# Kernel optimization log

Hardware: AMD Instinct MI355X
Metric: run time of the kernel (lower is better)

The kernel has to match this reference:

```python
import jax, jax.numpy as jnp
import numpy as np

NUM_TOKENS_SCORE = 64
NUM_HEADS = 16
NUM_KV_HEADS = 4
HEAD_SIZE = 128
SCALE = 0.08838834764831845  # 1/sqrt(128)


def setup_inputs() -> dict:
    key = jax.random.key(0)
    k1, k2, k3 = jax.random.split(key, 3)
    B, S = 2, 2048
    total = B * S
    return {
        "query": jax.random.normal(k1, (total, NUM_HEADS * HEAD_SIZE), dtype=jnp.float32),
        "key": jax.random.normal(k2, (total, NUM_KV_HEADS * HEAD_SIZE), dtype=jnp.float32),
        "value": jax.random.normal(k3, (total, NUM_KV_HEADS * HEAD_SIZE), dtype=jnp.float32),
        "batch_size": B,
        "seq_len": S,
    }


def reference(query, key, value, batch_size, seq_len):
    """Prompt-phase SparsePagedAttention: varlen causal GQA attention (equal
    prompt lengths -> dense [B,S] layout) plus the fused softmax score-sum over
    the last NUM_TOKENS_SCORE query rows used for KV-cache pruning."""
    B, S = batch_size, seq_len
    H, Hk, D = NUM_HEADS, NUM_KV_HEADS, HEAD_SIZE
    rep = H // Hk  # queries per kv head (head_mapping via repeat_interleave)

    q = query.reshape(B, S, H, D)
    k = jnp.repeat(key.reshape(B, S, Hk, D), rep, axis=2)    # [B,S,H,D]
    v = jnp.repeat(value.reshape(B, S, Hk, D), rep, axis=2)  # [B,S,H,D]

    scores = jnp.einsum('bqhd,bkhd->bhqk', q, k) * SCALE      # [B,H,S,S]
    causal = jnp.tril(jnp.ones((S, S), dtype=bool))
    scores = jnp.where(causal[None, None], scores, jnp.finfo(scores.dtype).min)
    probs = jax.nn.softmax(scores, axis=-1)                   # [B,H,S,S]

    out = jnp.einsum('bhqk,bkhd->bqhd', probs, v).reshape(B * S, H * D)
    # triton_fused_softmax_sum: sum softmax probs over last NUM_TOKENS_SCORE queries
    score_sum = probs[:, :, S - NUM_TOKENS_SCORE:, :].sum(axis=2)  # [B,H,S]
    return out, score_sum
```

## Files before the change

### kernel.cpp

```cpp
#include <hip/hip_runtime.h>


#define BB 2
#define SS 2048
#define NH 16
#define NKV 4
#define DD 128
#define TILE_SH 4096

typedef __attribute__((ext_vector_type(8))) short bf16x8;
typedef __attribute__((ext_vector_type(4))) float f32x4;

constexpr float SCL = 0.08838834764831845f * 1.4426950408889634f;

__device__ __forceinline__ short f2bf(float f) {
  union { float f; unsigned u; } v; v.f = f;
  unsigned r = v.u + 0x7FFFu + ((v.u >> 16) & 1u);
  return (short)(r >> 16);
}

__device__ __forceinline__ unsigned pack2bf(float a, float b) {
  union { float f; unsigned u; } x, y; x.f = a; y.f = b;
  return __builtin_amdgcn_perm(y.u, x.u, 0x07060302);
}

__device__ __forceinline__ void gl_lds16(const void* g, void* l) {
  __builtin_amdgcn_global_load_lds(
      (const __attribute__((address_space(1))) unsigned*)g,
      (__attribute__((address_space(3))) unsigned*)l, 16, 0, 0);
}

__global__ void prep(const float* __restrict__ K, const float* __restrict__ V,
                     short* __restrict__ Kb, short* __restrict__ Vb) {
  const int p = blockIdx.x;
  const int b = p >> 8, hk = (p >> 6) & 3, kt = p & 63;
  const int tid = threadIdx.x;
  const int k0 = kt * 32;
  short* kb = Kb + ((size_t)((b * 4 + hk) * 64 + kt)) * TILE_SH;
  short* vb = Vb + ((size_t)((b * 4 + hk) * 64 + kt)) * TILE_SH;
  {
    const int k = tid & 31, chb = tid >> 5;
    const float* src = K + ((size_t)(b * SS + k0 + k) * NKV + hk) * DD;
#pragma unroll
    for (int i = 0; i < 2; ++i) {
      const int ch = chb + i * 8;
      const float* s = src + ch * 8;
      float4 f0 = *(const float4*)s;
      float4 f1 = *(const float4*)(s + 4);
      bf16x8 t;
      t[0] = f2bf(f0.x); t[1] = f2bf(f0.y); t[2] = f2bf(f0.z); t[3] = f2bf(f0.w);
      t[4] = f2bf(f1.x); t[5] = f2bf(f1.y); t[6] = f2bf(f1.z); t[7] = f2bf(f1.w);
      *(bf16x8*)(kb + (ch * 32 + k) * 8) = t;
    }
  }
  {
    const int d = tid & 127, kcb = tid >> 7;
#pragma unroll
    for (int i = 0; i < 2; ++i) {
      const int kc = kcb + i * 2;
      const float* s = V + ((size_t)(b * SS + k0 + kc * 8) * NKV + hk) * DD + d;
      bf16x8 t;
#pragma unroll
      for (int e = 0; e < 8; ++e) t[e] = f2bf(s[(size_t)e * (NKV * DD)]);
      *(bf16x8*)(vb + (kc * 128 + d) * 8) = t;
    }
  }
}

__global__ __launch_bounds__(256, 4) void fa2(
    const float* __restrict__ Q, const short* __restrict__ Kb,
    const short* __restrict__ Vb, float* __restrict__ Out,
    float* __restrict__ wsl) {
  __shared__ bf16x8 kv[2][1024];
  __shared__ short ldsP[4][640];

  const int tid = threadIdx.x;
  const int w = tid >> 6, lane = tid & 63;
  const int c = lane & 15, qd = lane >> 4;

  const int i = blockIdx.x;
  const int g = i >> 8, cc = i & 255;
  const int bh = cc >> 3, jp = cc & 7;
  const int qt = (g == 0) ? jp : (g == 1) ? 31 - jp : (g == 2) ? 8 + jp : 23 - jp;
  const int b = bh >> 4, h = bh & 15, hk = h >> 2;

  const char* KT = (const char*)(Kb + ((size_t)(b * 4 + hk)) * 64 * TILE_SH);
  const char* VT = (const char*)(Vb + ((size_t)(b * 4 + hk)) * 64 * TILE_SH);

  auto stage = [&](int kt, int bi) {
    const char* sk = KT + (size_t)kt * 8192 + w * 2048 + lane * 16;
    const char* sv = VT + (size_t)kt * 8192 + w * 2048 + lane * 16;
    char* dk = (char*)kv[bi] + w * 2048;
    char* dv = dk + 8192;
#pragma unroll
    for (int t = 0; t < 2; ++t) {
      gl_lds16(sk + t * 1024, dk + t * 1024);
      gl_lds16(sv + t * 1024, dv + t * 1024);
    }
  };

  stage(0, 0);

  const int nk = 2 * qt + 2;

  const float* qrow = Q + ((size_t)(b * SS + qt * 64 + w * 16 + c) * NH + h) * DD;
  bf16x8 qf[4];
#pragma unroll
  for (int ks = 0; ks < 4; ++ks) {
    const float* p = qrow + ks * 32 + qd * 8;
    float4 f0 = *(const float4*)p;
    float4 f1 = *(const float4*)(p + 4);
    bf16x8 t;
    t[0] = f2bf(f0.x * SCL); t[1] = f2bf(f0.y * SCL);
    t[2] = f2bf(f0.z * SCL); t[3] = f2bf(f0.w * SCL);
    t[4] = f2bf(f1.x * SCL); t[5] = f2bf(f1.y * SCL);
    t[6] = f2bf(f1.z * SCL); t[7] = f2bf(f1.w * SCL);
    qf[ks] = t;
  }

  f32x4 o[8];
#pragma unroll
  for (int dt = 0; dt < 8; ++dt) { o[dt][0] = 0.f; o[dt][1] = 0.f; o[dt][2] = 0.f; o[dt][3] = 0.f; }
  float l_part = 0.f;

  for (int kt = 0; kt < nk; ++kt) {
    __syncthreads();
    const int cb = kt & 1;
    if (kt + 1 < nk) stage(kt + 1, cb ^ 1);

    const bf16x8* bK = kv[cb];
    const bf16x8* bV = kv[cb] + 512;

    f32x4 st0 = {0.f, 0.f, 0.f, 0.f}, st1 = {0.f, 0.f, 0.f, 0.f};
#pragma unroll
    for (int ks = 0; ks < 4; ++ks) {
      const int chz = (ks * 4 + qd) * 32;
      bf16x8 a0 = bK[chz + c];
      bf16x8 a1 = bK[chz + 16 + c];
      st0 = __builtin_amdgcn_mfma_f32_16x16x32_bf16(a0, qf[ks], st0, 0, 0, 0);
      st1 = __builtin_amdgcn_mfma_f32_16x16x32_bf16(a1, qf[ks], st1, 0, 0, 0);
    }

    float pr[8];
#pragma unroll
    for (int r = 0; r < 4; ++r) { pr[r] = exp2f(st0[r]); pr[4 + r] = exp2f(st1[r]); }
    const int koff = kt * 32 - qt * 64;
    if (koff >= 0) {
      const int qrl = w * 16 + c;
#pragma unroll
      for (int mt = 0; mt < 2; ++mt)
#pragma unroll
        for (int r = 0; r < 4; ++r)
          if (koff + mt * 16 + qd * 4 + r > qrl) pr[mt * 4 + r] = 0.f;
    }
#pragma unroll
    for (int x = 0; x < 8; ++x) l_part += pr[x];

    short* pp = ldsP[w] + c * 40;
#pragma unroll
    for (int mt = 0; mt < 2; ++mt) {
      union { short4 s4; unsigned u[2]; } pk;
      pk.u[0] = pack2bf(pr[mt * 4 + 0], pr[mt * 4 + 1]);
      pk.u[1] = pack2bf(pr[mt * 4 + 2], pr[mt * 4 + 3]);
      *(short4*)(pp + mt * 16 + qd * 4) = pk.s4;
    }
    __asm__ volatile("s_waitcnt lgkmcnt(0)" ::: "memory");
    bf16x8 pf = *(const bf16x8*)(pp + qd * 8);

#pragma unroll
    for (int dt = 0; dt < 8; ++dt)
      o[dt] = __builtin_amdgcn_mfma_f32_16x16x32_bf16(bV[qd * 128 + dt * 16 + c],
                                                      pf, o[dt], 0, 0, 0);
  }

  float l = l_part;
  l += __shfl_xor(l, 16);
  l += __shfl_xor(l, 32);
  const float linv = 1.f / l;

  float* orow = Out + ((size_t)(b * SS + qt * 64 + w * 16 + c) * NH + h) * DD;
#pragma unroll
  for (int dt = 0; dt < 8; ++dt) {
    float4 ov;
    ov.x = o[dt][0] * linv; ov.y = o[dt][1] * linv;
    ov.z = o[dt][2] * linv; ov.w = o[dt][3] * linv;
    *(float4*)(orow + dt * 16 + qd * 4) = ov;
  }
  if (qt == 31 && qd == 0)
    wsl[bh * 64 + w * 16 + c] = l;
}

__global__ __launch_bounds__(256, 2) void score(
    const float* __restrict__ Q, const short* __restrict__ Kb,
    const float* __restrict__ wsl, float* __restrict__ out2) {
  __shared__ float ldsS[4][64];
  const int tid = threadIdx.x;
  const int w = tid >> 6, lane = tid & 63;
  const int c = lane & 15, qd = lane >> 4;
  const int bh = blockIdx.x & 31, kt = blockIdx.x >> 5;
  const int b = bh >> 4, h = bh & 15, hk = h >> 2;
  const int q0 = SS - 64;

  const float* qrow = Q + ((size_t)(b * SS + q0 + w * 16 + c) * NH + h) * DD;
  bf16x8 qf[4];
#pragma unroll
  for (int ks = 0; ks < 4; ++ks) {
    const float* p = qrow + ks * 32 + qd * 8;
    float4 f0 = *(const float4*)p;
    float4 f1 = *(const float4*)(p + 4);
    bf16x8 t;
    t[0] = f2bf(f0.x * SCL); t[1] = f2bf(f0.y * SCL);
    t[2] = f2bf(f0.z * SCL); t[3] = f2bf(f0.w * SCL);
    t[4] = f2bf(f1.x * SCL); t[5] = f2bf(f1.y * SCL);
    t[6] = f2bf(f1.z * SCL); t[7] = f2bf(f1.w * SCL);
    qf[ks] = t;
  }
  float linv[4];
  const int r0 = bh * 64 + w * 16 + qd * 4;
#pragma unroll
  for (int r = 0; r < 4; ++r) linv[r] = 1.f / wsl[r0 + r];

  const bf16x8* kb = (const bf16x8*)Kb + ((size_t)(b * 4 + hk) * 64 + kt * 2) * 512;
  f32x4 s[4];
#pragma unroll
  for (int nt = 0; nt < 4; ++nt) { s[nt][0] = 0.f; s[nt][1] = 0.f; s[nt][2] = 0.f; s[nt][3] = 0.f; }
#pragma unroll
  for (int ks = 0; ks < 4; ++ks) {
#pragma unroll
    for (int nt = 0; nt < 4; ++nt) {
      bf16x8 kf = kb[(nt >> 1) * 512 + (ks * 4 + qd) * 32 + (nt & 1) * 16 + c];
      s[nt] = __builtin_amdgcn_mfma_f32_16x16x32_bf16(qf[ks], kf, s[nt], 0, 0, 0);
    }
  }
  const bool diag = (kt == 31);
  float cs[4] = {0.f, 0.f, 0.f, 0.f};
#pragma unroll
  for (int nt = 0; nt < 4; ++nt) {
#pragma unroll
    for (int r = 0; r < 4; ++r) {
      float pv = exp2f(s[nt][r]) * linv[r];
      if (diag && nt * 16 + c > w * 16 + qd * 4 + r) pv = 0.f;
      cs[nt] += pv;
    }
    cs[nt] += __shfl_xor(cs[nt], 16);
    cs[nt] += __shfl_xor(cs[nt], 32);
  }
  if (lane < 16) {
#pragma unroll
    for (int nt = 0; nt < 4; ++nt) ldsS[w][nt * 16 + c] = cs[nt];
  }
  __syncthreads();
  if (tid < 64)
    out2[(size_t)bh * SS + kt * 64 + tid] =
        ldsS[0][tid] + ldsS[1][tid] + ldsS[2][tid] + ldsS[3][tid];
}

extern "C" void kernel_launch(void* const* d_in, const int* in_sizes, int n_in,
                              void* d_out, int out_size, void* d_ws, size_t ws_size,
                              hipStream_t stream) {
  const float* Q = (const float*)d_in[0];
  const float* K = (const float*)d_in[1];
  const float* V = (const float*)d_in[2];
  float* out = (float*)d_out;
  float* out2 = out + (size_t)BB * SS * NH * DD;

  short* Kb = (short*)d_ws;
  const size_t tsz = (size_t)2 * 4 * 64 * TILE_SH;
  short* Vb = Kb + tsz;
  float* wsl = (float*)(Vb + tsz);

  hipLaunchKernelGGL(prep, dim3(512), dim3(256), 0, stream, K, V, Kb, Vb);
  hipLaunchKernelGGL(fa2, dim3(1024), dim3(256), 0, stream, Q, Kb, Vb, out, wsl);
  hipLaunchKernelGGL(score, dim3(1024), dim3(256), 0, stream, Q, Kb, wsl, out2);
}
```

Before: 160.6 us.

## Stage only K in LDS, load V fragments directly from global into registers

The attention kernel now stages only K tiles into LDS, two 32-key tiles per iteration. V fragments for the PV MFMA are read straight from global memory into registers, issued ahead of the QK compute to hide latency. This halves the number of block barriers per key range and removes the V traffic through LDS. In exchange it adds register pressure from holding 16 V fragments and depends on L2/global latency being hidden by the QK work.

```diff
diff --git a/kernel.cpp b/kernel.cpp
--- a/kernel.cpp
+++ b/kernel.cpp
@@ -87,23 +87,135 @@
   const char* KT = (const char*)(Kb + ((size_t)(b * 4 + hk)) * 64 * TILE_SH);
   const char* VT = (const char*)(Vb + ((size_t)(b * 4 + hk)) * 64 * TILE_SH);
 
-  auto stage = [&](int kt, int bi) {
-    const char* sk = KT + (size_t)kt * 8192 + w * 2048 + lane * 16;
-    const char* sv = VT + (size_t)kt * 8192 + w * 2048 + lane * 16;
-    char* dk = (char*)kv[bi] + w * 2048;
-    char* dv = dk + 8192;
-#pragma unroll
-    for (int t = 0; t < 2; ++t) {
-      gl_lds16(sk + t * 1024, dk + t * 1024);
-      gl_lds16(sv + t * 1024, dv + t * 1024);
-    }
+  auto stage = [&](int iv, int bi) {
+    const char* sk = KT + (size_t)iv * 16384 + w * 4096 + lane * 16;
+    char* dk = (char*)kv[bi] + w * 4096;
+#pragma unroll
+    for (int t = 0; t < 4; ++t) gl_lds16(sk + t * 1024, dk + t * 1024);
   };
 
   stage(0, 0);
 
-  const int nk = 2 * qt + 2;
-
   const float* qrow = Q + ((size_t)(b * SS + qt * 64 + w * 16 + c) * NH + h) * DD;
+  bf16x8 qf[4];
+#pragma unroll
+  for (int ks = 0; ks < 4; ++ks) {
+    const float* p = qrow + ks * 32 + qd * 8;
+    float4 f0 = *(const float4*)p;
+    float4 f1 = *(const float4*)(p + 4);
+    bf16x8 tq;
+    tq[0] = f2bf(f0.x * SCL); tq[1] = f2bf(f0.y * SCL);
+    tq[2] = f2bf(f0.z * SCL); tq[3] = f2bf(f0.w * SCL);
+    tq[4] = f2bf(f1.x * SCL); tq[5] = f2bf(f1.y * SCL);
+    tq[6] = f2bf(f1.z * SCL); tq[7] = f2bf(f1.w * SCL);
+    qf[ks] = tq;
+  }
+
+  f32x4 o[8];
+#pragma unroll
+  for (int dt = 0; dt < 8; ++dt) { o[dt][0] = 0.f; o[dt][1] = 0.f; o[dt][2] = 0.f; o[dt][3] = 0.f; }
+  float l_part = 0.f;
+
+  const int niv = qt + 1;
+
+  auto qkp = [&](const bf16x8* bKt, int kt) -> bf16x8 {
+    f32x4 st0 = {0.f, 0.f, 0.f, 0.f}, st1 = {0.f, 0.f, 0.f, 0.f};
+#pragma unroll
+    for (int ks = 0; ks < 4; ++ks) {
+      const int chz = (ks * 4 + qd) * 32;
+      bf16x8 a0 = bKt[chz + c];
+      bf16x8 a1 = bKt[chz + 16 + c];
+      st0 = __builtin_amdgcn_mfma_f32_16x16x32_bf16(a0, qf[ks], st0, 0, 0, 0);
+      st1 = __builtin_amdgcn_mfma_f32_16x16x32_bf16(a1, qf[ks], st1, 0, 0, 0);
+    }
+    float pr[8];
+#pragma unroll
+    for (int r = 0; r < 4; ++r) { pr[r] = exp2f(st0[r]); pr[4 + r] = exp2f(st1[r]); }
+    const int koff = kt * 32 - qt * 64;
+    if (koff >= 0) {
+      const int qrl = w * 16 + c;
+#pragma unroll
+      for (int mt = 0; mt < 2; ++mt)
+#pragma unroll
+        for (int r = 0; r < 4; ++r)
+          if (koff + mt * 16 + qd * 4 + r > qrl) pr[mt * 4 + r] = 0.f;
+    }
+#pragma unroll
+    for (int x = 0; x < 8; ++x) l_part += pr[x];
+
+    short* pp = ldsP[w] + c * 40;
+#pragma unroll
+    for (int mt = 0; mt < 2; ++mt) {
+      union { short4 s4; unsigned u[2]; } pk;
+      pk.u[0] = pack2bf(pr[mt * 4 + 0], pr[mt * 4 + 1]);
+      pk.u[1] = pack2bf(pr[mt * 4 + 2], pr[mt * 4 + 3]);
+      *(short4*)(pp + mt * 16 + qd * 4) = pk.s4;
+    }
+    __asm__ volatile("s_waitcnt lgkmcnt(0)" ::: "memory");
+    return *(const bf16x8*)(pp + qd * 8);
+  };
+
+  for (int iv = 0; iv < niv; ++iv) {
+    __syncthreads();
+    const int cb = iv & 1;
+    const bf16x8* bK = kv[cb];
+
+    bf16x8 av0[8];
+    const bf16x8* vg0 =
+        (const bf16x8*)(VT + (size_t)(2 * iv) * 8192) + (qd * 128 + c);
+#pragma unroll
+    for (int dt = 0; dt < 8; ++dt) av0[dt] = vg0[dt * 16];
+
+    bf16x8 pf0 = qkp(bK, 2 * iv);
+
+#pragma unroll
+    for (int dt = 0; dt < 8; ++dt)
+      o[dt] = __builtin_amdgcn_mfma_f32_16x16x32_bf16(av0[dt], pf0, o[dt], 0, 0, 0);
+
+    bf16x8 av1[8];
+    const bf16x8* vg1 =
+        (const bf16x8*)(VT + (size_t)(2 * iv + 1) * 8192) + (qd * 128 + c);
+#pragma unroll
+    for (int dt = 0; dt < 8; ++dt) av1[dt] = vg1[dt * 16];
+
+    if (iv + 1 < niv) stage(iv + 1, cb ^ 1);
+
+    bf16x8 pf1 = qkp(bK + 512, 2 * iv + 1);
+
+#pragma unroll
+    for (int dt = 0; dt < 8; ++dt)
+      o[dt] = __builtin_amdgcn_mfma_f32_16x16x32_bf16(av1[dt], pf1, o[dt], 0, 0, 0);
+  }
+
+  float l = l_part;
+  l += __shfl_xor(l, 16);
+  l += __shfl_xor(l, 32);
+  const float linv = 1.f / l;
+
+  float* orow = Out + ((size_t)(b * SS + qt * 64 + w * 16 + c) * NH + h) * DD;
+#pragma unroll
+  for (int dt = 0; dt < 8; ++dt) {
+    float4 ov;
+    ov.x = o[dt][0] * linv; ov.y = o[dt][1] * linv;
+    ov.z = o[dt][2] * linv; ov.w = o[dt][3] * linv;
+    *(float4*)(orow + dt * 16 + qd * 4) = ov;
+  }
+  if (qt == 31 && qd == 0)
+    wsl[bh * 64 + w * 16 + c] = l;
+}
+
+__global__ __launch_bounds__(256, 2) void score(
+    const float* __restrict__ Q, const short* __restrict__ Kb,
+    const float* __restrict__ wsl, float* __restrict__ out2) {
+  __shared__ float ldsS[4][64];
+  const int tid = threadIdx.x;
+  const int w = tid >> 6, lane = tid & 63;
+  const int c = lane & 15, qd = lane >> 4;
+  const int bh = blockIdx.x & 31, kt = blockIdx.x >> 5;
+  const int b = bh >> 4, h = bh & 15, hk = h >> 2;
+  const int q0 = SS - 64;
+
+  const float* qrow = Q + ((size_t)(b * SS + q0 + w * 16 + c) * NH + h) * DD;
   bf16x8 qf[4];
 #pragma unroll
   for (int ks = 0; ks < 4; ++ks) {
@@ -117,104 +229,6 @@
     t[6] = f2bf(f1.z * SCL); t[7] = f2bf(f1.w * SCL);
     qf[ks] = t;
   }
-
-  f32x4 o[8];
-#pragma unroll
-  for (int dt = 0; dt < 8; ++dt) { o[dt][0] = 0.f; o[dt][1] = 0.f; o[dt][2] = 0.f; o[dt][3] = 0.f; }
-  float l_part = 0.f;
-
-  for (int kt = 0; kt < nk; ++kt) {
-    __syncthreads();
-    const int cb = kt & 1;
-    if (kt + 1 < nk) stage(kt + 1, cb ^ 1);
-
-    const bf16x8* bK = kv[cb];
-    const bf16x8* bV = kv[cb] + 512;
-
-    f32x4 st0 = {0.f, 0.f, 0.f, 0.f}, st1 = {0.f, 0.f, 0.f, 0.f};
-#pragma unroll
-    for (int ks = 0; ks < 4; ++ks) {
-      const int chz = (ks * 4 + qd) * 32;
-      bf16x8 a0 = bK[chz + c];
-      bf16x8 a1 = bK[chz + 16 + c];
-      st0 = __builtin_amdgcn_mfma_f32_16x16x32_bf16(a0, qf[ks], st0, 0, 0, 0);
-      st1 = __builtin_amdgcn_mfma_f32_16x16x32_bf16(a1, qf[ks], st1, 0, 0, 0);
-    }
-
-    float pr[8];
-#pragma unroll
-    for (int r = 0; r < 4; ++r) { pr[r] = exp2f(st0[r]); pr[4 + r] = exp2f(st1[r]); }
-    const int koff = kt * 32 - qt * 64;
-    if (koff >= 0) {
-      const int qrl = w * 16 + c;
-#pragma unroll
-      for (int mt = 0; mt < 2; ++mt)
-#pragma unroll
-        for (int r = 0; r < 4; ++r)
-          if (koff + mt * 16 + qd * 4 + r > qrl) pr[mt * 4 + r] = 0.f;
-    }
-#pragma unroll
-    for (int x = 0; x < 8; ++x) l_part += pr[x];
-
-    short* pp = ldsP[w] + c * 40;
-#pragma unroll
-    for (int mt = 0; mt < 2; ++mt) {
-      union { short4 s4; unsigned u[2]; } pk;
-      pk.u[0] = pack2bf(pr[mt * 4 + 0], pr[mt * 4 + 1]);
-      pk.u[1] = pack2bf(pr[mt * 4 + 2], pr[mt * 4 + 3]);
-      *(short4*)(pp + mt * 16 + qd * 4) = pk.s4;
-    }
-    __asm__ volatile("s_waitcnt lgkmcnt(0)" ::: "memory");
-    bf16x8 pf = *(const bf16x8*)(pp + qd * 8);
-
-#pragma unroll
-    for (int dt = 0; dt < 8; ++dt)
-      o[dt] = __builtin_amdgcn_mfma_f32_16x16x32_bf16(bV[qd * 128 + dt * 16 + c],
-                                                      pf, o[dt], 0, 0, 0);
-  }
-
-  float l = l_part;
-  l += __shfl_xor(l, 16);
-  l += __shfl_xor(l, 32);
-  const float linv = 1.f / l;
-
-  float* orow = Out + ((size_t)(b * SS + qt * 64 + w * 16 + c) * NH + h) * DD;
-#pragma unroll
-  for (int dt = 0; dt < 8; ++dt) {
-    float4 ov;
-    ov.x = o[dt][0] * linv; ov.y = o[dt][1] * linv;
-    ov.z = o[dt][2] * linv; ov.w = o[dt][3] * linv;
-    *(float4*)(orow + dt * 16 + qd * 4) = ov;
-  }
-  if (qt == 31 && qd == 0)
-    wsl[bh * 64 + w * 16 + c] = l;
-}
-
-__global__ __launch_bounds__(256, 2) void score(
-    const float* __restrict__ Q, const short* __restrict__ Kb,
-    const float* __restrict__ wsl, float* __restrict__ out2) {
-  __shared__ float ldsS[4][64];
-  const int tid = threadIdx.x;
-  const int w = tid >> 6, lane = tid & 63;
-  const int c = lane & 15, qd = lane >> 4;
-  const int bh = blockIdx.x & 31, kt = blockIdx.x >> 5;
-  const int b = bh >> 4, h = bh & 15, hk = h >> 2;
-  const int q0 = SS - 64;
-
-  const float* qrow = Q + ((size_t)(b * SS + q0 + w * 16 + c) * NH + h) * DD;
-  bf16x8 qf[4];
-#pragma unroll
-  for (int ks = 0; ks < 4; ++ks) {
-    const float* p = qrow + ks * 32 + qd * 8;
-    float4 f0 = *(const float4*)p;
-    float4 f1 = *(const float4*)(p + 4);
-    bf16x8 t;
-    t[0] = f2bf(f0.x * SCL); t[1] = f2bf(f0.y * SCL);
-    t[2] = f2bf(f0.z * SCL); t[3] = f2bf(f0.w * SCL);
-    t[4] = f2bf(f1.x * SCL); t[5] = f2bf(f1.y * SCL);
-    t[6] = f2bf(f1.z * SCL); t[7] = f2bf(f1.w * SCL);
-    qf[ks] = t;
-  }
   float linv[4];
   const int r0 = bh * 64 + w * 16 + qd * 4;
 #pragma unroll
```

Result: no change. 159.3 us (-0.8%).
